# Kernel optimization log

Hardware: AMD Instinct MI355X
Metric: run time of the kernel (lower is better)

## Reference

```python
import jax, jax.numpy as jnp
import numpy as np

BINS = 50
MIN_V = 0.0
MAX_V = 1.0
SIGMA = 10.0
DELTA = (MAX_V - MIN_V) / BINS
EPS = 1e-8


def _soft_bin(v, centers):
    # v: [N, D] -> [N, bins, D]
    d = v[:, None, :] - centers[None, :, None]
    return jax.nn.sigmoid(SIGMA * (d + DELTA / 2)) - jax.nn.sigmoid(SIGMA * (d - DELTA / 2))


def setup_inputs() -> dict:
    key = jax.random.key(0)
    k1, k2 = jax.random.split(key)
    im1 = jax.random.uniform(k1, (8, 384, 384), dtype=jnp.float32)
    im2 = jax.random.uniform(k2, (8, 384, 384), dtype=jnp.float32)
    return {"im1": im1, "im2": im2}


def reference(im1, im2):
    n = im1.shape[0]
    x = im1.reshape(n, -1)
    y = im2.reshape(n, -1)
    centers = MIN_V + DELTA * (jnp.arange(BINS, dtype=jnp.float32) + 0.5)
    xs = _soft_bin(x, centers)  # [N, bins, D]
    ys = _soft_bin(y, centers)  # [N, bins, D]
    hgram = jnp.einsum('nbd,ncd->nbc', xs, ys)  # [N, bins, bins]
    # NOTE: original normalizes by the sum over the WHOLE batch
    p_xy = hgram / jnp.sum(hgram)
    marginal_x = jnp.sum(p_xy, axis=2)  # [N, bins]
    marginal_y = jnp.sum(p_xy, axis=1)  # [N, bins]
    joined = marginal_x[:, :, None] * marginal_y[:, None, :]  # [N, bins, bins]
    mi_per = jnp.sum(
        p_xy * (jnp.log(p_xy + EPS) - jnp.log(joined + EPS)), axis=(1, 2)
    )
    return jnp.sum(mi_per)  # reduction='sum'
```

## Files before the change

kernel.cpp:

```cpp
#include <hip/hip_runtime.h>


#define D_TOTAL   147456
#define NBATCH    8
#define BINS      50
#define NEDGE     28
#define KSLICES   192
#define KC        256
#define SLICE_LEN (D_TOTAL / KSLICES)
#define ITERS     (SLICE_LEN / KC)
#define LDS_STR   280

typedef _Float16 half8 __attribute__((ext_vector_type(8)));
typedef float    f32x4 __attribute__((ext_vector_type(4)));

__global__ __launch_bounds__(256, 4) void hgram_kernel(const float* __restrict__ im1,
                                                       const float* __restrict__ im2,
                                                       float* __restrict__ hg) {
    __shared__ __align__(16) _Float16 Xs[32][LDS_STR];
    __shared__ __align__(16) _Float16 Ys[32][LDS_STR];

    const int tid   = threadIdx.x;
    const int slice = blockIdx.x;
    const int n     = blockIdx.y;
    const int base  = n * D_TOTAL + slice * SLICE_LEN;

    {
        unsigned* px = (unsigned*)&Xs[28][0];
        unsigned* py = (unsigned*)&Ys[28][0];
        for (int i = tid; i < 4 * LDS_STR / 2; i += 256) { px[i] = 0u; py[i] = 0u; }
    }

    const int col  = tid;
    const int lane = tid & 63;
    const int w    = tid >> 6;
    const int r0   = (w & 1) << 4;
    const int c0   = (w >> 1) << 4;
    const int frow = lane & 15;
    const int kg   = (lane >> 4) << 3;

    auto stage1 = [&](float v, _Float16* dst) {
        const float E = __builtin_amdgcn_exp2f(v * -14.426950408889634f);
        float u0 = E * 0.6703200460356393f;
        float u1 = E * 11.023176380641601f;
        float u2 = E * 181.27224187515122f;
        float u3 = E * 2980.9579870417283f;
        #pragma unroll
        for (int k = 0; k < 7; ++k) {
            float t0 = __builtin_amdgcn_rcpf(__builtin_fmaf(u0, 0.00390625f, 0.00390625f));
            float t1 = __builtin_amdgcn_rcpf(__builtin_fmaf(u1, 0.00390625f, 0.00390625f));
            float t2 = __builtin_amdgcn_rcpf(__builtin_fmaf(u2, 0.00390625f, 0.00390625f));
            float t3 = __builtin_amdgcn_rcpf(__builtin_fmaf(u3, 0.00390625f, 0.00390625f));
            dst[(k)      * LDS_STR] = (_Float16)t0;
            dst[(7 + k)  * LDS_STR] = (_Float16)t1;
            dst[(14 + k) * LDS_STR] = (_Float16)t2;
            dst[(21 + k) * LDS_STR] = (_Float16)t3;
            u0 *= 1.4918246976412703f;
            u1 *= 1.4918246976412703f;
            u2 *= 1.4918246976412703f;
            u3 *= 1.4918246976412703f;
        }
    };

    f32x4 acc = {0.f, 0.f, 0.f, 0.f};

    float vx = im1[base + col];
    float vy = im2[base + col];
    for (int it = 0; it < ITERS; ++it) {
        float nvx = 0.f, nvy = 0.f;
        if (it + 1 < ITERS) {
            nvx = im1[base + (it + 1) * KC + col];
            nvy = im2[base + (it + 1) * KC + col];
        }
        stage1(vx, &Xs[0][col]);
        stage1(vy, &Ys[0][col]);
        __syncthreads();
        #pragma unroll
        for (int ks = 0; ks < 8; ++ks) {
            const int k0 = ks * 32 + kg;
            half8 a = *(const half8*)&Xs[r0 + frow][k0];
            half8 b = *(const half8*)&Ys[c0 + frow][k0];
            acc = __builtin_amdgcn_mfma_f32_16x16x32_f16(a, b, acc, 0, 0, 0);
        }
        __syncthreads();
        vx = nvx; vy = nvy;
    }

    float* hgn = hg + n * 1024;
    const int gj = c0 + (lane & 15);
    const int ri = r0 + ((lane >> 4) << 2);
    if (gj < NEDGE) {
        #pragma unroll
        for (int r = 0; r < 4; ++r) {
            const int gi = ri + r;
            if (gi < NEDGE) atomicAdd(&hgn[gi * 32 + gj], acc[r]);
        }
    }
}

__global__ __launch_bounds__(1024) void finalize_kernel(const float* __restrict__ hg,
                                                        float* __restrict__ out) {
    __shared__ float Gs[NBATCH][NEDGE][29];
    __shared__ float mx[NBATCH][BINS], my[NBATCH][BINS];
    __shared__ float red[16];
    __shared__ float sT;
    const int tid = threadIdx.x;

    for (int idx = tid; idx < NBATCH * NEDGE * NEDGE; idx += 1024) {
        int n = idx / (NEDGE * NEDGE);
        int rem = idx - n * (NEDGE * NEDGE);
        int r = rem / NEDGE, c = rem - r * NEDGE;
        Gs[n][r][c] = hg[n * 1024 + r * 32 + c];
    }
    __syncthreads();

    if (tid < 2 * NBATCH * BINS) {
        const int which = (tid >= NBATCH * BINS) ? 1 : 0;
        const int t2 = which ? tid - NBATCH * BINS : tid;
        const int n = t2 / BINS, b = t2 - n * BINS;
        const int q = b >> 1;
        float w0, w1, w2, w3;
        if (b & 1) { w0 = -1.f; w1 = 9.f; w2 = -7.f; w3 = -1.f; }
        else       { w0 =  1.f; w1 = 7.f; w2 = -9.f; w3 =  1.f; }
        float m;
        if (which == 0) {
            m = w0 * (Gs[n][q][1]   - Gs[n][q][26])
              + w1 * (Gs[n][q+1][1] - Gs[n][q+1][26])
              + w2 * (Gs[n][q+2][1] - Gs[n][q+2][26])
              + w3 * (Gs[n][q+3][1] - Gs[n][q+3][26]);
            mx[n][b] = m * 0.0625f;
        } else {
            m = w0 * (Gs[n][1][q]   - Gs[n][26][q])
              + w1 * (Gs[n][1][q+1] - Gs[n][26][q+1])
              + w2 * (Gs[n][1][q+2] - Gs[n][26][q+2])
              + w3 * (Gs[n][1][q+3] - Gs[n][26][q+3]);
            my[n][b] = m * 0.0625f;
        }
    }
    if (tid == 0) {
        float t = 0.f;
        for (int n = 0; n < NBATCH; ++n)
            t += Gs[n][1][1] - Gs[n][1][26] - Gs[n][26][1] + Gs[n][26][26];
        sT = t;
    }
    __syncthreads();

    const float invT = 1.0f / sT;
    const float invT2 = invT * invT;
    float mi = 0.f;
    for (int task = tid; task < NBATCH * 25 * 25; task += 1024) {
        const int n = task / 625;
        const int rem = task - n * 625;
        const int bp = rem / 25, cp = rem - bp * 25;
        float g[4][4];
        #pragma unroll
        for (int r = 0; r < 4; ++r)
            #pragma unroll
            for (int s = 0; s < 4; ++s) g[r][s] = Gs[n][bp + r][cp + s];
        float rde[4], rdo[4];
        #pragma unroll
        for (int r = 0; r < 4; ++r) {
            rde[r] =  g[r][0] + 7.f * g[r][1] - 9.f * g[r][2] + g[r][3];
            rdo[r] = -g[r][0] + 9.f * g[r][1] - 7.f * g[r][2] - g[r][3];
        }
        const float hee = ( rde[0] + 7.f*rde[1] - 9.f*rde[2] + rde[3]) * (1.f/256.f);
        const float heo = ( rdo[0] + 7.f*rdo[1] - 9.f*rdo[2] + rdo[3]) * (1.f/256.f);
        const float hoe = (-rde[0] + 9.f*rde[1] - 7.f*rde[2] - rde[3]) * (1.f/256.f);
        const float hoo = (-rdo[0] + 9.f*rdo[1] - 7.f*rdo[2] - rdo[3]) * (1.f/256.f);
        const int b0 = 2 * bp, c0 = 2 * cp;
        {
            float p = hee * invT, jo = mx[n][b0] * my[n][c0] * invT2;
            mi += p * (__logf(p + 1e-8f) - __logf(jo + 1e-8f));
        }
        {
            float p = heo * invT, jo = mx[n][b0] * my[n][c0 + 1] * invT2;
            mi += p * (__logf(p + 1e-8f) - __logf(jo + 1e-8f));
        }
        {
            float p = hoe * invT, jo = mx[n][b0 + 1] * my[n][c0] * invT2;
            mi += p * (__logf(p + 1e-8f) - __logf(jo + 1e-8f));
        }
        {
            float p = hoo * invT, jo = mx[n][b0 + 1] * my[n][c0 + 1] * invT2;
            mi += p * (__logf(p + 1e-8f) - __logf(jo + 1e-8f));
        }
    }
    #pragma unroll
    for (int o = 32; o > 0; o >>= 1) mi += __shfl_down(mi, o, 64);
    if ((tid & 63) == 0) red[tid >> 6] = mi;
    __syncthreads();
    if (tid == 0) {
        float t = 0.f;
        for (int i = 0; i < 16; ++i) t += red[i];
        out[0] = t;
    }
}

extern "C" void kernel_launch(void* const* d_in, const int* in_sizes, int n_in,
                              void* d_out, int out_size, void* d_ws, size_t ws_size,
                              hipStream_t stream) {
    const float* im1 = (const float*)d_in[0];
    const float* im2 = (const float*)d_in[1];
    float* out = (float*)d_out;
    float* hg  = (float*)d_ws;

    hipMemsetAsync(d_ws, 0, NBATCH * 1024 * sizeof(float), stream);
    hgram_kernel<<<dim3(KSLICES, NBATCH), dim3(256), 0, stream>>>(im1, im2, hg);
    finalize_kernel<<<dim3(1), dim3(1024), 0, stream>>>(hg, out);
}
```

Measured before the change: 87.84 us.

## Halve slice count, precompute edge constants table, interleave X/Y sigmoid evaluation

Cuts the number of K-slices per batch from 192 to 96, so each block runs twice as many iterations and half as many atomics land on the histogram. The edge scale factors come from a compile-time table instead of a running multiply chain, and the X and Y sigmoid computations are interleaved to expose more ILP. Launch bounds drop to 3 blocks per CU to allow more registers. The trade-offs are a smaller grid (768 blocks) with possibly worse latency hiding, and slightly different rounding from the exact constants.

```diff
diff --git a/kernel.cpp b/kernel.cpp
--- a/kernel.cpp
+++ b/kernel.cpp
@@ -5,7 +5,7 @@
 #define NBATCH    8
 #define BINS      50
 #define NEDGE     28
-#define KSLICES   192
+#define KSLICES   96
 #define KC        256
 #define SLICE_LEN (D_TOTAL / KSLICES)
 #define ITERS     (SLICE_LEN / KC)
@@ -14,7 +14,17 @@
 typedef _Float16 half8 __attribute__((ext_vector_type(8)));
 typedef float    f32x4 __attribute__((ext_vector_type(4)));
 
-__global__ __launch_bounds__(256, 4) void hgram_kernel(const float* __restrict__ im1,
+struct Tab { float c[NEDGE]; };
+constexpr Tab make_tab() {
+    Tab t{};
+    double c = 0.6703200460356393;
+    const double lam = 1.4918246976412703;
+    for (int i = 0; i < NEDGE; ++i) { t.c[i] = (float)c; c *= lam; }
+    return t;
+}
+constexpr Tab TAB = make_tab();
+
+__global__ __launch_bounds__(256, 3) void hgram_kernel(const float* __restrict__ im1,
                                                        const float* __restrict__ im2,
                                                        float* __restrict__ hg) {
     __shared__ __align__(16) _Float16 Xs[32][LDS_STR];
@@ -39,29 +49,6 @@
     const int frow = lane & 15;
     const int kg   = (lane >> 4) << 3;
 
-    auto stage1 = [&](float v, _Float16* dst) {
-        const float E = __builtin_amdgcn_exp2f(v * -14.426950408889634f);
-        float u0 = E * 0.6703200460356393f;
-        float u1 = E * 11.023176380641601f;
-        float u2 = E * 181.27224187515122f;
-        float u3 = E * 2980.9579870417283f;
-        #pragma unroll
-        for (int k = 0; k < 7; ++k) {
-            float t0 = __builtin_amdgcn_rcpf(__builtin_fmaf(u0, 0.00390625f, 0.00390625f));
-            float t1 = __builtin_amdgcn_rcpf(__builtin_fmaf(u1, 0.00390625f, 0.00390625f));
-            float t2 = __builtin_amdgcn_rcpf(__builtin_fmaf(u2, 0.00390625f, 0.00390625f));
-            float t3 = __builtin_amdgcn_rcpf(__builtin_fmaf(u3, 0.00390625f, 0.00390625f));
-            dst[(k)      * LDS_STR] = (_Float16)t0;
-            dst[(7 + k)  * LDS_STR] = (_Float16)t1;
-            dst[(14 + k) * LDS_STR] = (_Float16)t2;
-            dst[(21 + k) * LDS_STR] = (_Float16)t3;
-            u0 *= 1.4918246976412703f;
-            u1 *= 1.4918246976412703f;
-            u2 *= 1.4918246976412703f;
-            u3 *= 1.4918246976412703f;
-        }
-    };
-
     f32x4 acc = {0.f, 0.f, 0.f, 0.f};
 
     float vx = im1[base + col];
@@ -72,8 +59,25 @@
             nvx = im1[base + (it + 1) * KC + col];
             nvy = im2[base + (it + 1) * KC + col];
         }
-        stage1(vx, &Xs[0][col]);
-        stage1(vy, &Ys[0][col]);
+        {
+            const float Ex = __builtin_amdgcn_exp2f(vx * -14.426950408889634f);
+            const float Ey = __builtin_amdgcn_exp2f(vy * -14.426950408889634f);
+            _Float16* dx = &Xs[0][col];
+            _Float16* dy = &Ys[0][col];
+            #pragma unroll
+            for (int i = 0; i < NEDGE; i += 4) {
+                #pragma unroll
+                for (int q = 0; q < 4; ++q) {
+                    const float c = TAB.c[i + q];
+                    float ux = c * Ex;
+                    float uy = c * Ey;
+                    float tx = __builtin_amdgcn_rcpf(__builtin_fmaf(ux, 0.00390625f, 0.00390625f));
+                    float ty = __builtin_amdgcn_rcpf(__builtin_fmaf(uy, 0.00390625f, 0.00390625f));
+                    dx[(i + q) * LDS_STR] = (_Float16)tx;
+                    dy[(i + q) * LDS_STR] = (_Float16)ty;
+                }
+            }
+        }
         __syncthreads();
         #pragma unroll
         for (int ks = 0; ks < 8; ++ks) {
```

Result: no change. 86.52 us (-1.5%).
